# Optimization experiments

Measured on AMD Instinct MI355X. Metric: run time of the kernel, lower is better.

The kernel has to match this reference:

```python
import jax, jax.numpy as jnp
import numpy as np

B, T = 32, 48
INPUT_DIM = 40000
TRAJ = 10
H = 256
OUT = 40000
TD = 48
L = 2
E = 128
DIN = E + TD  # 176


def setup_inputs() -> dict:
    key = jax.random.key(0)
    ks = jax.random.split(key, 16)
    s = 0.05
    inp = {
        "locations": jax.random.randint(ks[0], (B, T), 0, INPUT_DIM),
        "times": jax.random.randint(ks[1], (B, T), 0, TD),
        "labels": jax.random.randint(ks[2], (B,), 0, TRAJ),
        "embed_table": jax.random.normal(ks[3], (INPUT_DIM, E), dtype=jnp.float32) * s,
        "traj_table": jax.random.normal(ks[4], (TRAJ, H * L), dtype=jnp.float32) * s,
        "fc_w": jax.random.normal(ks[5], (OUT + TD, H), dtype=jnp.float32) * s,
        "fc_b": jnp.zeros((OUT + TD,), dtype=jnp.float32),
        "w_ih0": jax.random.normal(ks[6], (3 * H, DIN), dtype=jnp.float32) * s,
        "w_hh0": jax.random.normal(ks[7], (3 * H, H), dtype=jnp.float32) * s,
        "b_ih0": jnp.zeros((3 * H,), dtype=jnp.float32),
        "b_hh0": jnp.zeros((3 * H,), dtype=jnp.float32),
        "w_ih1": jax.random.normal(ks[8], (3 * H, H), dtype=jnp.float32) * s,
        "w_hh1": jax.random.normal(ks[9], (3 * H, H), dtype=jnp.float32) * s,
        "b_ih1": jnp.zeros((3 * H,), dtype=jnp.float32),
        "b_hh1": jnp.zeros((3 * H,), dtype=jnp.float32),
    }
    return inp


def gru_layer(x, h0, w_ih, w_hh, b_ih, b_hh):
    """PyTorch-semantics GRU layer. x: [T,B,din], h0: [B,H] -> [T,B,H]."""
    # precompute input projections for all timesteps (gates ordered r,z,n)
    xp = jnp.einsum('tbd,gd->tbg', x, w_ih) + b_ih  # [T,B,3H]

    def step(h, xp_t):
        hp = h @ w_hh.T + b_hh                      # [B,3H]
        xr, xz, xn = jnp.split(xp_t, 3, axis=-1)
        hr, hz, hn = jnp.split(hp, 3, axis=-1)
        r = jax.nn.sigmoid(xr + hr)
        z = jax.nn.sigmoid(xz + hz)
        n = jnp.tanh(xn + r * hn)
        h_new = (1.0 - z) * n + z * h
        return h_new, h_new

    _, ys = jax.lax.scan(step, h0, xp)
    return ys


def reference(locations, times, labels, embed_table, traj_table, fc_w, fc_b,
              w_ih0, w_hh0, b_ih0, b_hh0, w_ih1, w_hh1, b_ih1, b_hh1):
    x = embed_table[locations]                                  # [B,T,E]
    th = jax.nn.one_hot(times, TD, dtype=x.dtype)               # [B,T,TD]
    x = jnp.concatenate([x, th], axis=-1).transpose(1, 0, 2)    # [T,B,E+TD]
    # init_hidden: view (B, L*H) -> (L, -1, H), a raw reshape as in torch
    h0 = traj_table[labels].reshape(L, -1, H)                   # [L,B,H]
    y = gru_layer(x, h0[0], w_ih0, w_hh0, b_ih0, b_hh0)
    y = gru_layer(y, h0[1], w_ih1, w_hh1, b_ih1, b_hh1)         # [T,B,H]
    out = jax.nn.relu(y).transpose(1, 0, 2) @ fc_w.T + fc_b     # [B,T,OUT+TD]
    loc = jax.nn.log_softmax(out[..., :OUT], axis=-1)
    tm = jax.nn.log_softmax(out[..., OUT:], axis=-1)
    return loc, tm
```

## Files before the change

### kernel.cpp

```cpp
#include <hip/hip_runtime.h>
#include <math.h>

typedef __attribute__((ext_vector_type(4))) float f32x4;
typedef __attribute__((ext_vector_type(8))) short s16x8;

constexpr int B = 32, T = 48, H = 256, E = 128, TD = 48;
constexpr int OUT = 40000, NOUTC = 40048, NPADC = 40064;
constexpr int G3 = 768, DIN = 176;
constexpr int NT = 313, NTP = 320;

__device__ __forceinline__ float sigmoidf_(float x){ return 1.f/(1.f+__expf(-x)); }
__device__ __forceinline__ float tanhf_(float x){
  float e = __expf(2.f*x);
  return 1.f - 2.f/(e + 1.f);
}
__device__ __forceinline__ unsigned short f2bf(float f){
  unsigned int u = __float_as_uint(f);
  u += 0x7fffu + ((u>>16)&1u);
  return (unsigned short)(u>>16);
}
__device__ __forceinline__ s16x8 pack8(float4 u, float4 v){
  s16x8 r;
  r[0]=(short)f2bf(u.x); r[1]=(short)f2bf(u.y); r[2]=(short)f2bf(u.z); r[3]=(short)f2bf(u.w);
  r[4]=(short)f2bf(v.x); r[5]=(short)f2bf(v.y); r[6]=(short)f2bf(v.z); r[7]=(short)f2bf(v.w);
  return r;
}
__device__ __forceinline__ void gl_lds16(const unsigned short* g, unsigned short* l){
  __builtin_amdgcn_global_load_lds((const __attribute__((address_space(1))) void*)g,
                                   (__attribute__((address_space(3))) void*)l, 16, 0, 0);
}
__device__ __forceinline__ void st_sc(unsigned* p, unsigned v){
  __hip_atomic_store(p, v, __ATOMIC_RELAXED, __HIP_MEMORY_SCOPE_SYSTEM);
}
__device__ __forceinline__ unsigned ld_sc32(const unsigned* p){
  return __hip_atomic_load((unsigned*)p, __ATOMIC_RELAXED, __HIP_MEMORY_SCOPE_SYSTEM);
}
__device__ __forceinline__ unsigned long long ld_sc64(const unsigned long long* p){
  return __hip_atomic_load((unsigned long long*)p, __ATOMIC_RELAXED, __HIP_MEMORY_SCOPE_SYSTEM);
}

__global__ void wt_kernel(const float* __restrict__ w_ih0, float* __restrict__ wT,
                          unsigned* __restrict__ flags){
  int i = blockIdx.x*256 + threadIdx.x;
  if (blockIdx.x == 0 && threadIdx.x < 32)
    __hip_atomic_store(&flags[threadIdx.x], 0u, __ATOMIC_RELAXED, __HIP_MEMORY_SCOPE_SYSTEM);
  if (i >= E*G3) return;
  int e = i / G3, g = i % G3;
  wT[i] = w_ih0[g*DIN + e];
}

__global__ void xp0_kernel(const int* __restrict__ locations, const int* __restrict__ times,
                           const float* __restrict__ embed, const float* __restrict__ wT,
                           const float* __restrict__ w_ih0, const float* __restrict__ b_ih0,
                           float* __restrict__ xp0)
{
  __shared__ float emb_s[16][E];
  __shared__ int tm_s[16];
  const int r0 = blockIdx.x * 16;
  const int tid = threadIdx.x;
  for (int i = tid; i < 16*E; i += 256) {
    int p = i >> 7, e = i & 127;
    int r = r0 + p; int t = r >> 5, b = r & 31;
    emb_s[p][e] = embed[(size_t)locations[b*T + t]*E + e];
  }
  if (tid < 16) {
    int r = r0 + tid; int t = r >> 5, b = r & 31;
    tm_s[tid] = times[b*T + t];
  }
  __syncthreads();
  const int g = tid;
  float acc[16][3];
  #pragma unroll
  for (int p=0;p<16;p++){acc[p][0]=0.f;acc[p][1]=0.f;acc[p][2]=0.f;}
  for (int e = 0; e < E; e += 4) {
    float w0_[4], w1_[4], w2_[4];
    #pragma unroll
    for (int i=0;i<4;i++){
      w0_[i]=wT[(e+i)*G3 + g];
      w1_[i]=wT[(e+i)*G3 + 256 + g];
      w2_[i]=wT[(e+i)*G3 + 512 + g];
    }
    #pragma unroll
    for (int p=0;p<16;p++){
      float4 ev = *(const float4*)&emb_s[p][e];
      acc[p][0] += ev.x*w0_[0]+ev.y*w0_[1]+ev.z*w0_[2]+ev.w*w0_[3];
      acc[p][1] += ev.x*w1_[0]+ev.y*w1_[1]+ev.z*w1_[2]+ev.w*w1_[3];
      acc[p][2] += ev.x*w2_[0]+ev.y*w2_[1]+ev.z*w2_[2]+ev.w*w2_[3];
    }
  }
  #pragma unroll
  for (int p=0;p<16;p++){
    int r = r0+p; int tt = tm_s[p];
    xp0[(size_t)r*G3 + g]       = acc[p][0] + b_ih0[g]     + w_ih0[g*DIN       + E + tt];
    xp0[(size_t)r*G3 + 256 + g] = acc[p][1] + b_ih0[g+256] + w_ih0[(g+256)*DIN + E + tt];
    xp0[(size_t)r*G3 + 512 + g] = acc[p][2] + b_ih0[g+512] + w_ih0[(g+512)*DIN + E + tt];
  }
}

struct GruArgs {
  const float* xp0; const float* traj; const int* labels;
  const float* w_hh0; const float* b_hh0;
  const float* w_ih1; const float* w_hh1; const float* b_ih1; const float* b_hh1;
  unsigned* exch;
  unsigned* flags;
  unsigned short* abf;
};

__global__ void __launch_bounds__(384, 2) gru_kernel(GruArgs a)
{
  __shared__ unsigned short Ash[2][32*264];
  __shared__ float gl0[3*32*17];
  __shared__ float gl1[4*32*17];
  const int tid  = threadIdx.x;
  const int jt   = blockIdx.x;
  const int wv   = tid >> 6;
  const int lane = tid & 63;
  const int g    = wv % 3, mt = wv / 3;
  const int fn   = lane & 15;
  const int fq   = lane >> 4;

  const int row = g*256 + jt*16 + fn;
  s16x8 b0[8], b1[16];
  #pragma unroll
  for (int kk = 0; kk < 8; ++kk) {
    const float* p0 = a.w_hh0 + (size_t)row*H + kk*32 + fq*8;
    const float* p1 = a.w_ih1 + (size_t)row*H + kk*32 + fq*8;
    const float* p2 = a.w_hh1 + (size_t)row*H + kk*32 + fq*8;
    b0[kk]    = pack8(*(const float4*)p0, *(const float4*)(p0+4));
    b1[kk]    = pack8(*(const float4*)p1, *(const float4*)(p1+4));
    b1[kk+8]  = pack8(*(const float4*)p2, *(const float4*)(p2+4));
  }

  const int pb = tid >> 3, pjp = tid & 7, pj0 = pjp*2, pgj = jt*16 + pj0;
  float2 bh0r, bh0z, bh0n, bi1r, bi1z, bi1n, bh1r, bh1z, bh1n;
  float hc00 = 0.f, hc01 = 0.f, hc10 = 0.f, hc11 = 0.f;
  if (tid < 256) {
    bh0r = *(const float2*)&a.b_hh0[pgj];
    bh0z = *(const float2*)&a.b_hh0[256+pgj];
    bh0n = *(const float2*)&a.b_hh0[512+pgj];
    bi1r = *(const float2*)&a.b_ih1[pgj];
    bi1z = *(const float2*)&a.b_ih1[256+pgj];
    bi1n = *(const float2*)&a.b_ih1[512+pgj];
    bh1r = *(const float2*)&a.b_hh1[pgj];
    bh1z = *(const float2*)&a.b_hh1[256+pgj];
    bh1n = *(const float2*)&a.b_hh1[512+pgj];
  }

  for (int i = tid; i < 2*B*H; i += 384) {
    int l = i >> 13, bb = (i >> 8) & 31, h = i & 255;
    float v = a.traj[(size_t)a.labels[l*16 + (bb>>1)]*512 + (bb&1)*256 + h];
    Ash[l][bb*264 + h] = f2bf(v);
  }
  if (tid < 256) {
    float v00 = a.traj[(size_t)a.labels[(pb>>1)]*512      + (pb&1)*256 + pgj];
    float v01 = a.traj[(size_t)a.labels[(pb>>1)]*512      + (pb&1)*256 + pgj+1];
    float v10 = a.traj[(size_t)a.labels[16 + (pb>>1)]*512 + (pb&1)*256 + pgj];
    float v11 = a.traj[(size_t)a.labels[16 + (pb>>1)]*512 + (pb&1)*256 + pgj+1];
    hc00 = v00; hc01 = v01; hc10 = v10; hc11 = v11;
    st_sc(&a.exch[1*8192 + ((jt*2 + 1)*32 + pb)*8 + pjp],
          (unsigned)f2bf(v10) | ((unsigned)f2bf(v11) << 16));
  }

  for (int p = 0; p <= T; ++p) {
    float2 xr, xz, xn;
    if (p < T && tid < 256) {
      const float* xp = a.xp0 + (size_t)(p*B + pb)*G3 + pgj;
      xr = *(const float2*)(xp);
      xz = *(const float2*)(xp + 256);
      xn = *(const float2*)(xp + 512);
    }
    if (p) {
      const unsigned want = (unsigned)p;
      {
        unsigned it = 0;
        for (;;) {
          unsigned f = want;
          if (lane < 16) f = ld_sc32(&a.flags[(p & 1)*16 + lane]);
          if (__all((int)(f >= want))) break;
          if (++it > (1u << 22)) break;
        }
      }
      const unsigned long long* src = (const unsigned long long*)a.exch + (size_t)(p & 1)*4096;
      unsigned long long v[11];
      #pragma unroll
      for (int k = 0; k < 11; ++k) {
        int i = tid + k*384;
        if (i < 4096) v[k] = ld_sc64(&src[i]);
      }
      #pragma unroll
      for (int k = 0; k < 11; ++k) {
        int i = tid + k*384;
        if (i < 4096) {
          int pp = i & 3, bb = (i >> 2) & 31, st = (i >> 7) & 1, jtp = (i >> 8) & 15;
          *(unsigned long long*)&Ash[st][bb*264 + jtp*16 + pp*4] = v[k];
        }
      }
    }
    __syncthreads();

    if (p < T) {
      f32x4 acc = (f32x4){0.f,0.f,0.f,0.f};
      #pragma unroll
      for (int kk = 0; kk < 8; ++kk) {
        s16x8 af = *(const s16x8*)&Ash[0][(mt*16 + fn)*264 + kk*32 + fq*8];
        acc = __builtin_amdgcn_mfma_f32_16x16x32_bf16(af, b0[kk], acc, 0, 0, 0);
      }
      #pragma unroll
      for (int i = 0; i < 4; ++i)
        gl0[(g*32 + mt*16 + fq*4 + i)*17 + fn] = acc[i];
    }
    if (p >= 1) {
      if (g < 2) {
        f32x4 acc = (f32x4){0.f,0.f,0.f,0.f};
        #pragma unroll
        for (int kk = 0; kk < 8; ++kk) {
          s16x8 af = *(const s16x8*)&Ash[0][(mt*16 + fn)*264 + kk*32 + fq*8];
          acc = __builtin_amdgcn_mfma_f32_16x16x32_bf16(af, b1[kk], acc, 0, 0, 0);
        }
        #pragma unroll
        for (int kk = 0; kk < 8; ++kk) {
          s16x8 af = *(const s16x8*)&Ash[1][(mt*16 + fn)*264 + kk*32 + fq*8];
          acc = __builtin_amdgcn_mfma_f32_16x16x32_bf16(af, b1[8+kk], acc, 0, 0, 0);
        }
        #pragma unroll
        for (int i = 0; i < 4; ++i)
          gl1[(g*32 + mt*16 + fq*4 + i)*17 + fn] = acc[i];
      } else {
        f32x4 ax = (f32x4){0.f,0.f,0.f,0.f}, ah = (f32x4){0.f,0.f,0.f,0.f};
        #pragma unroll
        for (int kk = 0; kk < 8; ++kk) {
          s16x8 afx = *(const s16x8*)&Ash[0][(mt*16 + fn)*264 + kk*32 + fq*8];
          s16x8 afh = *(const s16x8*)&Ash[1][(mt*16 + fn)*264 + kk*32 + fq*8];
          ax = __builtin_amdgcn_mfma_f32_16x16x32_bf16(afx, b1[kk],   ax, 0, 0, 0);
          ah = __builtin_amdgcn_mfma_f32_16x16x32_bf16(afh, b1[8+kk], ah, 0, 0, 0);
        }
        #pragma unroll
        for (int i = 0; i < 4; ++i) {
          gl1[(2*32 + mt*16 + fq*4 + i)*17 + fn] = ax[i];
          gl1[(3*32 + mt*16 + fq*4 + i)*17 + fn] = ah[i];
        }
      }
    }
    __syncthreads();

    if (tid < 256) {
      const int slot = (p + 1) & 1;
      if (p < T) {
        float r0 = sigmoidf_(xr.x + gl0[pb*17+pj0]        + bh0r.x);
        float r1 = sigmoidf_(xr.y + gl0[pb*17+pj0+1]      + bh0r.y);
        float z0 = sigmoidf_(xz.x + gl0[(32+pb)*17+pj0]   + bh0z.x);
        float z1 = sigmoidf_(xz.y + gl0[(32+pb)*17+pj0+1] + bh0z.y);
        float n0 = tanhf_(xn.x + r0*(gl0[(64+pb)*17+pj0]   + bh0n.x));
        float n1 = tanhf_(xn.y + r1*(gl0[(64+pb)*17+pj0+1] + bh0n.y));
        float h0n = (1.f - z0)*n0 + z0*hc00;
        float h1n = (1.f - z1)*n1 + z1*hc01;
        hc00 = h0n; hc01 = h1n;
        st_sc(&a.exch[(size_t)slot*8192 + ((jt*2 + 0)*32 + pb)*8 + pjp],
              (unsigned)f2bf(h0n) | ((unsigned)f2bf(h1n) << 16));
      }
      if (p >= 1) {
        const int t1 = p - 1;
        float r0 = sigmoidf_(gl1[pb*17+pj0]        + bi1r.x + bh1r.x);
        float r1 = sigmoidf_(gl1[pb*17+pj0+1]      + bi1r.y + bh1r.y);
        float z0 = sigmoidf_(gl1[(32+pb)*17+pj0]   + bi1z.x + bh1z.x);
        float z1 = sigmoidf_(gl1[(32+pb)*17+pj0+1] + bi1z.y + bh1z.y);
        float n0 = tanhf_(gl1[(64+pb)*17+pj0]   + bi1n.x + r0*(gl1[(96+pb)*17+pj0]   + bh1n.x));
        float n1 = tanhf_(gl1[(64+pb)*17+pj0+1] + bi1n.y + r1*(gl1[(96+pb)*17+pj0+1] + bh1n.y));
        float h0n = (1.f - z0)*n0 + z0*hc10;
        float h1n = (1.f - z1)*n1 + z1*hc11;
        hc10 = h0n; hc11 = h1n;
        if (p < T)
          st_sc(&a.exch[(size_t)slot*8192 + ((jt*2 + 1)*32 + pb)*8 + pjp],
                (unsigned)f2bf(h0n) | ((unsigned)f2bf(h1n) << 16));
        ((unsigned*)a.abf)[((size_t)(pb*T + t1)*H + pgj) >> 1] =
              (unsigned)f2bf(fmaxf(h0n,0.f)) | ((unsigned)f2bf(fmaxf(h1n,0.f)) << 16);
      }
    }
    if (p < T) {
      asm volatile("s_waitcnt vmcnt(0)" ::: "memory");
      __syncthreads();
      if (tid == 0)
        st_sc(&a.flags[((p + 1) & 1)*16 + jt], (unsigned)(p + 1));
    }
  }
}

__global__ void castw_kernel(const float* __restrict__ fcw, unsigned short* __restrict__ wbf){
  int g = blockIdx.x*256 + threadIdx.x;
  if (g >= NPADC*64) return;
  int row = g >> 6;
  ushort4 o;
  if (row < NOUTC) {
    float4 v = ((const float4*)fcw)[g];
    o.x=f2bf(v.x); o.y=f2bf(v.y); o.z=f2bf(v.z); o.w=f2bf(v.w);
  } else { o.x=0; o.y=0; o.z=0; o.w=0; }
  ((ushort4*)wbf)[g] = o;
}

__global__ void __launch_bounds__(256) gemm_kernel(const unsigned short* __restrict__ Abf,
                                                   const unsigned short* __restrict__ Wbf,
                                                   const float* __restrict__ fc_b,
                                                   float* __restrict__ dout,
                                                   float2* __restrict__ part)
{
  __shared__ unsigned short As[128*32];
  __shared__ unsigned short Ws[128*32];
  const int m0 = blockIdx.x * 128;
  const int n0 = blockIdx.y * 128;
  const int tid = threadIdx.x;
  const int lane = tid & 63;
  const int wv = tid >> 6;
  f32x4 acc[2][8];
  #pragma unroll
  for (int i=0;i<2;i++)
    #pragma unroll
    for(int jx=0;jx<8;jx++) acc[i][jx] = (f32x4){0.f,0.f,0.f,0.f};

  const int srow = tid >> 2;
  const int skoff = (tid & 3) * 8;
  const unsigned short* aptr = Abf + (size_t)(m0 + srow)*256 + skoff;
  const unsigned short* wptr = Wbf + (size_t)(n0 + srow)*256 + skoff;
  unsigned short* asd = &As[tid*8];
  unsigned short* wsd = &Ws[tid*8];

  const int fr = lane & 15;
  const int fk = (lane >> 4) * 8;

  for (int kk = 0; kk < 256; kk += 32) {
    gl_lds16(aptr + kk,            asd);
    gl_lds16(aptr + 64*256 + kk,   asd + 64*32);
    gl_lds16(wptr + kk,            wsd);
    gl_lds16(wptr + 64*256 + kk,   wsd + 64*32);
    __syncthreads();
    s16x8 a0 = *(const s16x8*)&As[(wv*32 + fr)*32 + fk];
    s16x8 a1 = *(const s16x8*)&As[(wv*32 + 16 + fr)*32 + fk];
    #pragma unroll
    for (int ct = 0; ct < 8; ++ct) {
      s16x8 bfr = *(const s16x8*)&Ws[(ct*16 + fr)*32 + fk];
      acc[0][ct] = __builtin_amdgcn_mfma_f32_16x16x32_bf16(a0, bfr, acc[0][ct], 0, 0, 0);
      acc[1][ct] = __builtin_amdgcn_mfma_f32_16x16x32_bf16(a1, bfr, acc[1][ct], 0, 0, 0);
    }
    __syncthreads();
  }

  const int quad = lane >> 4;
  #pragma unroll
  for (int rt = 0; rt < 2; ++rt) {
    #pragma unroll
    for (int ct = 0; ct < 8; ++ct) {
      int col = n0 + ct*16 + fr;
      float bias = (col < NOUTC) ? fc_b[col] : 0.f;
      #pragma unroll
      for (int i = 0; i < 4; ++i) acc[rt][ct][i] += bias;
      if (col < NOUTC) {
        #pragma unroll
        for (int i = 0; i < 4; ++i) {
          int row2 = m0 + wv*32 + rt*16 + quad*4 + i;
          float v = acc[rt][ct][i];
          if (col < OUT) dout[(size_t)row2*OUT + col] = v;
          else dout[(size_t)OUT*B*T + (size_t)row2*TD + (col - OUT)] = v;
        }
      }
    }
  }
  #pragma unroll
  for (int rt = 0; rt < 2; ++rt) {
    #pragma unroll
    for (int i = 0; i < 4; ++i) {
      float mx = -INFINITY;
      #pragma unroll
      for (int ct = 0; ct < 8; ++ct)
        if (n0 + ct*16 + fr < OUT) mx = fmaxf(mx, acc[rt][ct][i]);
      #pragma unroll
      for (int off = 1; off < 16; off <<= 1) mx = fmaxf(mx, __shfl_xor(mx, off));
      float sx = 0.f;
      #pragma unroll
      for (int ct = 0; ct < 8; ++ct)
        if (n0 + ct*16 + fr < OUT) sx += __expf(acc[rt][ct][i] - mx);
      #pragma unroll
      for (int off = 1; off < 16; off <<= 1) sx += __shfl_xor(sx, off);
      if (fr == 0) {
        int row2 = m0 + wv*32 + rt*16 + quad*4 + i;
        part[(size_t)row2*NTP + (n0 >> 7)] = make_float2(mx, sx);
      }
    }
  }
}

__global__ void stats_kernel(const float2* __restrict__ part, float* __restrict__ logz){
  const int r = blockIdx.x;
  const int lane = threadIdx.x;
  float m = -INFINITY, s = 0.f;
  for (int i = lane; i < NT; i += 64) {
    float2 pp = part[(size_t)r*NTP + i];
    float nm = fmaxf(m, pp.x);
    s = s*__expf(m - nm) + pp.y*__expf(pp.x - nm);
    m = nm;
  }
  #pragma unroll
  for (int off = 1; off < 64; off <<= 1) {
    float m2 = __shfl_xor(m, off);
    float s2 = __shfl_xor(s, off);
    float nm = fmaxf(m, m2);
    s = s*__expf(m - nm) + s2*__expf(m2 - nm);
    m = nm;
  }
  if (lane == 0) logz[r] = m + logf(s);
}

__global__ void norm_kernel(float* __restrict__ dout, const float* __restrict__ logz){
  size_t i = (size_t)blockIdx.x*256 + threadIdx.x;
  if (i >= (size_t)B*T*OUT/4) return;
  int r = (int)(i / (OUT/4));
  float lz = logz[r];
  float4* p = (float4*)dout + i;
  float4 v = *p;
  v.x -= lz; v.y -= lz; v.z -= lz; v.w -= lz;
  *p = v;
}

__global__ void tm_kernel(float* __restrict__ dout){
  const int r = blockIdx.x;
  const int lane = threadIdx.x;
  float* base = dout + (size_t)OUT*B*T + (size_t)r*TD;
  float v = (lane < TD) ? base[lane] : -INFINITY;
  float m = v;
  #pragma unroll
  for (int off=32; off; off>>=1) m = fmaxf(m, __shfl_xor(m, off));
  float e = (lane < TD) ? __expf(v - m) : 0.f;
  float s = e;
  #pragma unroll
  for (int off=32; off; off>>=1) s += __shfl_xor(s, off);
  float lz = m + logf(s);
  if (lane < TD) base[lane] = v - lz;
}

extern "C" void kernel_launch(void* const* d_in, const int* in_sizes, int n_in,
                              void* d_out, int out_size, void* d_ws, size_t ws_size,
                              hipStream_t stream)
{
  const int*   locations = (const int*)d_in[0];
  const int*   times     = (const int*)d_in[1];
  const int*   labels    = (const int*)d_in[2];
  const float* embed     = (const float*)d_in[3];
  const float* traj      = (const float*)d_in[4];
  const float* fc_w      = (const float*)d_in[5];
  const float* fc_b      = (const float*)d_in[6];
  const float* w_ih0     = (const float*)d_in[7];
  const float* w_hh0     = (const float*)d_in[8];
  const float* b_ih0     = (const float*)d_in[9];
  const float* b_hh0     = (const float*)d_in[10];
  const float* w_ih1     = (const float*)d_in[11];
  const float* w_hh1     = (const float*)d_in[12];
  const float* b_ih1     = (const float*)d_in[13];
  const float* b_hh1     = (const float*)d_in[14];
  float* out = (float*)d_out;
  char* ws = (char*)d_ws;

  float* xp0            = (float*)(ws);
  float2* part          = (float2*)(ws);
  unsigned* exch        = (unsigned*)(ws + 4718592);
  unsigned* flags       = (unsigned*)(ws + 4784128);
  float* logz           = (float*)(ws + 4784384);
  unsigned short* abf   = (unsigned short*)(ws + 4790528);
  unsigned short* wbf   = (unsigned short*)(ws + 5576960);
  float* wT             = (float*)(ws + 26089728);

  castw_kernel<<<dim3((NPADC*64 + 255)/256), dim3(256), 0, stream>>>(fc_w, wbf);
  wt_kernel<<<dim3((E*G3 + 255)/256), dim3(256), 0, stream>>>(w_ih0, wT, flags);
  xp0_kernel<<<dim3(96), dim3(256), 0, stream>>>(locations, times, embed, wT, w_ih0, b_ih0, xp0);

  GruArgs ga{xp0, traj, labels, w_hh0, b_hh0, w_ih1, w_hh1, b_ih1, b_hh1,
             exch, flags, abf};
  void* kargs[] = { &ga };
  hipLaunchCooperativeKernel((void*)gru_kernel, dim3(16), dim3(384), kargs, 0, stream);

  gemm_kernel<<<dim3(12, 313), dim3(256), 0, stream>>>(abf, wbf, fc_b, out, part);
  stats_kernel<<<dim3(B*T), dim3(64), 0, stream>>>(part, logz);
  norm_kernel<<<dim3((B*T*OUT/4 + 255)/256), dim3(256), 0, stream>>>(out, logz);
  tm_kernel<<<dim3(B*T), dim3(64), 0, stream>>>(out);
}
```

Measured before the change: 720.2 us.

## Recompute FC GEMM in second pass to fuse log-softmax normalization, double-buffer LDS

The old flow wrote the full 1536x40000 logits, then the norm kernel read and rewrote them. Now the GEMM runs twice: the first pass emits only the per-tile max/sum partials, and the second recomputes the logits and writes them with logz already subtracted. This removes one full read-modify-write of roughly 245MB of output in exchange for a second GEMM. The GEMM also gains double-buffered LDS staging, and the GRU's relu output store is moved after the flag publish.

Result: no change. 719.4 us (-0.1%).

```diff
diff --git a/kernel.cpp b/kernel.cpp
--- a/kernel.cpp
+++ b/kernel.cpp
@@ -243,6 +243,7 @@
     }
     __syncthreads();
 
+    float relu0 = 0.f, relu1 = 0.f;
     if (tid < 256) {
       const int slot = (p + 1) & 1;
       if (p < T) {
@@ -259,7 +260,6 @@
               (unsigned)f2bf(h0n) | ((unsigned)f2bf(h1n) << 16));
       }
       if (p >= 1) {
-        const int t1 = p - 1;
         float r0 = sigmoidf_(gl1[pb*17+pj0]        + bi1r.x + bh1r.x);
         float r1 = sigmoidf_(gl1[pb*17+pj0+1]      + bi1r.y + bh1r.y);
         float z0 = sigmoidf_(gl1[(32+pb)*17+pj0]   + bi1z.x + bh1z.x);
@@ -272,8 +272,7 @@
         if (p < T)
           st_sc(&a.exch[(size_t)slot*8192 + ((jt*2 + 1)*32 + pb)*8 + pjp],
                 (unsigned)f2bf(h0n) | ((unsigned)f2bf(h1n) << 16));
-        ((unsigned*)a.abf)[((size_t)(pb*T + t1)*H + pgj) >> 1] =
-              (unsigned)f2bf(fmaxf(h0n,0.f)) | ((unsigned)f2bf(fmaxf(h1n,0.f)) << 16);
+        relu0 = fmaxf(h0n, 0.f); relu1 = fmaxf(h1n, 0.f);
       }
     }
     if (p < T) {
@@ -281,6 +280,10 @@
       __syncthreads();
       if (tid == 0)
         st_sc(&a.flags[((p + 1) & 1)*16 + jt], (unsigned)(p + 1));
+    }
+    if (p >= 1 && tid < 256) {
+      ((unsigned*)a.abf)[((size_t)(pb*T + (p - 1))*H + pgj) >> 1] =
+            (unsigned)f2bf(relu0) | ((unsigned)f2bf(relu1) << 16);
     }
   }
 }
@@ -297,14 +300,16 @@
   ((ushort4*)wbf)[g] = o;
 }
 
-__global__ void __launch_bounds__(256) gemm_kernel(const unsigned short* __restrict__ Abf,
-                                                   const unsigned short* __restrict__ Wbf,
-                                                   const float* __restrict__ fc_b,
-                                                   float* __restrict__ dout,
-                                                   float2* __restrict__ part)
+template <int WRITE>
+__global__ void __launch_bounds__(256) fc_kernel(const unsigned short* __restrict__ Abf,
+                                                 const unsigned short* __restrict__ Wbf,
+                                                 const float* __restrict__ fc_b,
+                                                 const float* __restrict__ logz,
+                                                 float* __restrict__ dout,
+                                                 float2* __restrict__ part)
 {
-  __shared__ unsigned short As[128*32];
-  __shared__ unsigned short Ws[128*32];
+  __shared__ unsigned short As[2][128*32];
+  __shared__ unsigned short Ws[2][128*32];
   const int m0 = blockIdx.x * 128;
   const int n0 = blockIdx.y * 128;
   const int tid = threadIdx.x;
@@ -320,27 +325,36 @@
   const int skoff = (tid & 3) * 8;
   const unsigned short* aptr = Abf + (size_t)(m0 + srow)*256 + skoff;
   const unsigned short* wptr = Wbf + (size_t)(n0 + srow)*256 + skoff;
-  unsigned short* asd = &As[tid*8];
-  unsigned short* wsd = &Ws[tid*8];
 
   const int fr = lane & 15;
   const int fk = (lane >> 4) * 8;
 
-  for (int kk = 0; kk < 256; kk += 32) {
-    gl_lds16(aptr + kk,            asd);
-    gl_lds16(aptr + 64*256 + kk,   asd + 64*32);
-    gl_lds16(wptr + kk,            wsd);
-    gl_lds16(wptr + 64*256 + kk,   wsd + 64*32);
-    __syncthreads();
-    s16x8 a0 = *(const s16x8*)&As[(wv*32 + fr)*32 + fk];
-    s16x8 a1 = *(const s16x8*)&As[(wv*32 + 16 + fr)*32 + fk];
+  auto stage = [&](int kc, int bb) {
+    unsigned short* asd = &As[bb][tid*8];
+    unsigned short* wsd = &Ws[bb][tid*8];
+    gl_lds16(aptr + kc*32,          asd);
+    gl_lds16(aptr + 64*256 + kc*32, asd + 64*32);
+    gl_lds16(wptr + kc*32,          wsd);
+    gl_lds16(wptr + 64*256 + kc*32, wsd + 64*32);
+  };
+
+  stage(0, 0);
+  asm volatile("s_waitcnt vmcnt(0)" ::: "memory");
+  __syncthreads();
+  int cur = 0;
+  for (int kc = 0; kc < 8; ++kc) {
+    if (kc < 7) stage(kc + 1, cur ^ 1);
+    s16x8 a0 = *(const s16x8*)&As[cur][(wv*32 + fr)*32 + fk];
+    s16x8 a1 = *(const s16x8*)&As[cur][(wv*32 + 16 + fr)*32 + fk];
     #pragma unroll
     for (int ct = 0; ct < 8; ++ct) {
-      s16x8 bfr = *(const s16x8*)&Ws[(ct*16 + fr)*32 + fk];
+      s16x8 bfr = *(const s16x8*)&Ws[cur][(ct*16 + fr)*32 + fk];
       acc[0][ct] = __builtin_amdgcn_mfma_f32_16x16x32_bf16(a0, bfr, acc[0][ct], 0, 0, 0);
       acc[1][ct] = __builtin_amdgcn_mfma_f32_16x16x32_bf16(a1, bfr, acc[1][ct], 0, 0, 0);
     }
+    asm volatile("s_waitcnt vmcnt(0)" ::: "memory");
     __syncthreads();
+    cur ^= 1;
   }
 
   const int quad = lane >> 4;
@@ -352,36 +366,46 @@
       float bias = (col < NOUTC) ? fc_b[col] : 0.f;
       #pragma unroll
       for (int i = 0; i < 4; ++i) acc[rt][ct][i] += bias;
-      if (col < NOUTC) {
-        #pragma unroll
-        for (int i = 0; i < 4; ++i) {
+    }
+  }
+
+  if (WRITE) {
+    #pragma unroll
+    for (int rt = 0; rt < 2; ++rt) {
+      #pragma unroll
+      for (int i = 0; i < 4; ++i) {
+        int row2 = m0 + wv*32 + rt*16 + quad*4 + i;
+        float lz = logz[row2];
+        #pragma unroll
+        for (int ct = 0; ct < 8; ++ct) {
+          int col = n0 + ct*16 + fr;
+          if (col < OUT) dout[(size_t)row2*OUT + col] = acc[rt][ct][i] - lz;
+          else if (col < NOUTC)
+            dout[(size_t)OUT*B*T + (size_t)row2*TD + (col - OUT)] = acc[rt][ct][i];
+        }
+      }
+    }
+  } else {
+    #pragma unroll
+    for (int rt = 0; rt < 2; ++rt) {
+      #pragma unroll
+      for (int i = 0; i < 4; ++i) {
+        float mx = -INFINITY;
+        #pragma unroll
+        for (int ct = 0; ct < 8; ++ct)
+          if (n0 + ct*16 + fr < OUT) mx = fmaxf(mx, acc[rt][ct][i]);
+        #pragma unroll
+        for (int off = 1; off < 16; off <<= 1) mx = fmaxf(mx, __shfl_xor(mx, off));
+        float sx = 0.f;
+        #pragma unroll
+        for (int ct = 0; ct < 8; ++ct)
+          if (n0 + ct*16 + fr < OUT) sx += __expf(acc[rt][ct][i] - mx);
+        #pragma unroll
+        for (int off = 1; off < 16; off <<= 1) sx += __shfl_xor(sx, off);
+        if (fr == 0) {
           int row2 = m0 + wv*32 + rt*16 + quad*4 + i;
-          float v = acc[rt][ct][i];
-          if (col < OUT) dout[(size_t)row2*OUT + col] = v;
-          else dout[(size_t)OUT*B*T + (size_t)row2*TD + (col - OUT)] = v;
-        }
-      }
-    }
-  }
-  #pragma unroll
-  for (int rt = 0; rt < 2; ++rt) {
-    #pragma unroll
-    for (int i = 0; i < 4; ++i) {
-      float mx = -INFINITY;
-      #pragma unroll
-      for (int ct = 0; ct < 8; ++ct)
-        if (n0 + ct*16 + fr < OUT) mx = fmaxf(mx, acc[rt][ct][i]);
-      #pragma unroll
-      for (int off = 1; off < 16; off <<= 1) mx = fmaxf(mx, __shfl_xor(mx, off));
-      float sx = 0.f;
-      #pragma unroll
-      for (int ct = 0; ct < 8; ++ct)
-        if (n0 + ct*16 + fr < OUT) sx += __expf(acc[rt][ct][i] - mx);
-      #pragma unroll
-      for (int off = 1; off < 16; off <<= 1) sx += __shfl_xor(sx, off);
-      if (fr == 0) {
-        int row2 = m0 + wv*32 + rt*16 + quad*4 + i;
-        part[(size_t)row2*NTP + (n0 >> 7)] = make_float2(mx, sx);
+          part[(size_t)row2*NTP + (n0 >> 7)] = make_float2(mx, sx);
+        }
       }
     }
   }
@@ -406,17 +430,6 @@
     m = nm;
   }
   if (lane == 0) logz[r] = m + logf(s);
-}
-
-__global__ void norm_kernel(float* __restrict__ dout, const float* __restrict__ logz){
-  size_t i = (size_t)blockIdx.x*256 + threadIdx.x;
-  if (i >= (size_t)B*T*OUT/4) return;
-  int r = (int)(i / (OUT/4));
-  float lz = logz[r];
-  float4* p = (float4*)dout + i;
-  float4 v = *p;
-  v.x -= lz; v.y -= lz; v.z -= lz; v.w -= lz;
-  *p = v;
 }
 
 __global__ void tm_kernel(float* __restrict__ dout){
@@ -475,8 +488,8 @@
   void* kargs[] = { &ga };
   hipLaunchCooperativeKernel((void*)gru_kernel, dim3(16), dim3(384), kargs, 0, stream);
 
-  gemm_kernel<<<dim3(12, 313), dim3(256), 0, stream>>>(abf, wbf, fc_b, out, part);
+  fc_kernel<0><<<dim3(12, 313), dim3(256), 0, stream>>>(abf, wbf, fc_b, nullptr, nullptr, part);
   stats_kernel<<<dim3(B*T), dim3(64), 0, stream>>>(part, logz);
-  norm_kernel<<<dim3((B*T*OUT/4 + 255)/256), dim3(256), 0, stream>>>(out, logz);
+  fc_kernel<1><<<dim3(12, 313), dim3(256), 0, stream>>>(abf, wbf, fc_b, logz, out, nullptr);
   tm_kernel<<<dim3(B*T), dim3(64), 0, stream>>>(out);
 }
```
